# Optimization experiments

Hardware: AMD Instinct MI355X
Metric: run time of the kernel (lower is better)

## Reference

```python
import jax, jax.numpy as jnp
import numpy as np

N_NODES = 50000
N_EDGES = 500000
H_DIM = 128
BN_EPS = 1e-5


def setup_inputs() -> dict:
    key = jax.random.key(0)
    k1, k2, k3, k4 = jax.random.split(key, 4)
    ent_emb = jax.random.normal(k1, (N_NODES, H_DIM), dtype=jnp.float32)
    neigh_w = jax.random.normal(k2, (H_DIM, H_DIM), dtype=jnp.float32) * 0.05
    gamma = jnp.ones((H_DIM,), dtype=jnp.float32)
    beta = jnp.zeros((H_DIM,), dtype=jnp.float32)
    src = jax.random.randint(k3, (N_EDGES,), 0, N_NODES, dtype=jnp.int32)
    dst = jax.random.randint(k4, (N_EDGES,), 0, N_NODES, dtype=jnp.int32)
    return {"ent_emb": ent_emb, "neigh_w": neigh_w, "gamma": gamma,
            "beta": beta, "src": src, "dst": dst}


def reference(ent_emb, neigh_w, gamma, beta, src, dst):
    # u_dot_v: per-edge dot product of src and dst node embeddings -> [E]
    e_src = ent_emb[src]                      # [E, D] gather
    scores = jnp.sum(e_src * ent_emb[dst], axis=-1)  # [E]

    # edge_softmax: softmax over incoming edges of each destination node
    seg_max = jax.ops.segment_max(scores, dst, num_segments=N_NODES)
    seg_max = jnp.where(jnp.isfinite(seg_max), seg_max, 0.0)  # empty nodes
    ex = jnp.exp(scores - seg_max[dst])
    denom = jax.ops.segment_sum(ex, dst, num_segments=N_NODES)
    norm = ex / denom[dst]                    # [E]

    # u_mul_e + sum: weighted scatter-sum of src embeddings into dst nodes
    neigh = jax.ops.segment_sum(e_src * norm[:, None], dst,
                                num_segments=N_NODES)  # [N, D]

    # linear + BatchNorm1d (training mode, batch stats) + tanh
    h = neigh @ neigh_w
    mu = jnp.mean(h, axis=0)
    var = jnp.var(h, axis=0)                  # biased, matches torch BN
    h = (h - mu) * jax.lax.rsqrt(var + BN_EPS) * gamma + beta
    return jnp.tanh(h)
```

## Files before the change

### kernel.cpp

```cpp
#include <hip/hip_runtime.h>
#include <hip/hip_bf16.h>
#include <math.h>

#define N_NODES 50000
#define N_EDGES 500000
#define H_DIM   128
#define BN_EPS  1e-5f
#define GEMM_GRID ((N_NODES + 31) / 32)
#define SCAN_NBLK ((N_NODES + 255) / 256)
#define RED_NBLK  64

__global__ __launch_bounds__(256) void hist_kernel(
    const int* __restrict__ dst, int* __restrict__ deg)
{
    int e = blockIdx.x * blockDim.x + threadIdx.x;
    if (e < N_EDGES) atomicAdd(&deg[dst[e]], 1);
}

__global__ __launch_bounds__(256) void scan_partial_kernel(
    const int* __restrict__ deg, int* __restrict__ blocksum)
{
    __shared__ int red[256];
    int t = threadIdx.x;
    int i = blockIdx.x * 256 + t;
    red[t] = (i < N_NODES) ? deg[i] : 0;
    __syncthreads();
    #pragma unroll
    for (int off = 128; off; off >>= 1) {
        if (t < off) red[t] += red[t + off];
        __syncthreads();
    }
    if (t == 0) blocksum[blockIdx.x] = red[0];
}

__global__ __launch_bounds__(256) void scan_final_kernel(
    const int* __restrict__ deg, const int* __restrict__ blocksum,
    int* __restrict__ rowptr, int* __restrict__ cursor)
{
    __shared__ int bs[256];
    __shared__ int s[256];
    int t = threadIdx.x;

    bs[t] = (t < SCAN_NBLK) ? blocksum[t] : 0;
    __syncthreads();
    for (int off = 1; off < 256; off <<= 1) {
        int v = (t >= off) ? bs[t - off] : 0;
        __syncthreads();
        bs[t] += v;
        __syncthreads();
    }
    int blockoff = (blockIdx.x == 0) ? 0 : bs[blockIdx.x - 1];

    int i = blockIdx.x * 256 + t;
    int v = (i < N_NODES) ? deg[i] : 0;
    s[t] = v;
    __syncthreads();
    for (int off = 1; off < 256; off <<= 1) {
        int u = (t >= off) ? s[t - off] : 0;
        __syncthreads();
        s[t] += u;
        __syncthreads();
    }
    int excl = s[t] - v + blockoff;
    if (i < N_NODES) {
        rowptr[i] = excl;
        cursor[i] = excl;
        if (i == N_NODES - 1) rowptr[N_NODES] = excl + v;
    }
}

__global__ __launch_bounds__(256) void csr_scatter_kernel(
    const int* __restrict__ src, const int* __restrict__ dst,
    int* __restrict__ cursor, int* __restrict__ csr_src)
{
    int e = blockIdx.x * blockDim.x + threadIdx.x;
    if (e >= N_EDGES) return;
    int pos = atomicAdd(&cursor[dst[e]], 1);
    csr_src[pos] = src[e];
}

__global__ __launch_bounds__(256) void node_aggregate_kernel(
    const float* __restrict__ emb,
    const int* __restrict__ rowptr,
    const int* __restrict__ csr_src,
    float* __restrict__ neigh)
{
    int node = blockIdx.x * 8 + (threadIdx.x >> 5);
    int lane = threadIdx.x & 31;
    if (node >= N_NODES) return;

    int beg = rowptr[node];
    int end = rowptr[node + 1];

    const float4 b = *((const float4*)(emb + (size_t)node * H_DIM) + lane);

    float m = -INFINITY;
    float denom = 0.f;
    float4 acc = {0.f, 0.f, 0.f, 0.f};

    int e = beg;

    for (; e + 8 <= end; e += 8) {
        float4 a[8];
        float  p[8];
        #pragma unroll
        for (int u = 0; u < 8; ++u) {
            int s = csr_src[e + u];
            a[u] = *((const float4*)(emb + (size_t)s * H_DIM) + lane);
        }
        #pragma unroll
        for (int u = 0; u < 8; ++u)
            p[u] = a[u].x * b.x + a[u].y * b.y + a[u].z * b.z + a[u].w * b.w;
        #pragma unroll
        for (int off = 16; off; off >>= 1) {
            #pragma unroll
            for (int u = 0; u < 8; ++u)
                p[u] += __shfl_xor(p[u], off);
        }
        float mn = m;
        #pragma unroll
        for (int u = 0; u < 8; ++u) mn = fmaxf(mn, p[u]);
        float corr = __expf(m - mn);
        float w[8];
        #pragma unroll
        for (int u = 0; u < 8; ++u) w[u] = __expf(p[u] - mn);
        float ws = 0.f;
        #pragma unroll
        for (int u = 0; u < 8; ++u) ws += w[u];
        denom = denom * corr + ws;
        float sx = 0.f, sy = 0.f, sz = 0.f, sw = 0.f;
        #pragma unroll
        for (int u = 0; u < 8; ++u) {
            sx += a[u].x * w[u];
            sy += a[u].y * w[u];
            sz += a[u].z * w[u];
            sw += a[u].w * w[u];
        }
        acc.x = acc.x * corr + sx;
        acc.y = acc.y * corr + sy;
        acc.z = acc.z * corr + sz;
        acc.w = acc.w * corr + sw;
        m = mn;
    }

    if (e + 4 <= end) {
        float4 a[4];
        float  p[4];
        #pragma unroll
        for (int u = 0; u < 4; ++u) {
            int s = csr_src[e + u];
            a[u] = *((const float4*)(emb + (size_t)s * H_DIM) + lane);
        }
        #pragma unroll
        for (int u = 0; u < 4; ++u)
            p[u] = a[u].x * b.x + a[u].y * b.y + a[u].z * b.z + a[u].w * b.w;
        #pragma unroll
        for (int off = 16; off; off >>= 1) {
            #pragma unroll
            for (int u = 0; u < 4; ++u)
                p[u] += __shfl_xor(p[u], off);
        }
        float mn = fmaxf(fmaxf(fmaxf(p[0], p[1]), fmaxf(p[2], p[3])), m);
        float corr = __expf(m - mn);
        float w[4];
        #pragma unroll
        for (int u = 0; u < 4; ++u) w[u] = __expf(p[u] - mn);
        denom = denom * corr + w[0] + w[1] + w[2] + w[3];
        acc.x = acc.x * corr + a[0].x*w[0] + a[1].x*w[1] + a[2].x*w[2] + a[3].x*w[3];
        acc.y = acc.y * corr + a[0].y*w[0] + a[1].y*w[1] + a[2].y*w[2] + a[3].y*w[3];
        acc.z = acc.z * corr + a[0].z*w[0] + a[1].z*w[1] + a[2].z*w[2] + a[3].z*w[3];
        acc.w = acc.w * corr + a[0].w*w[0] + a[1].w*w[1] + a[2].w*w[2] + a[3].w*w[3];
        m = mn;
        e += 4;
    }

    for (; e < end; ++e) {
        int s = csr_src[e];
        float4 a = *((const float4*)(emb + (size_t)s * H_DIM) + lane);
        float p = a.x * b.x + a.y * b.y + a.z * b.z + a.w * b.w;
        #pragma unroll
        for (int off = 16; off; off >>= 1)
            p += __shfl_xor(p, off);
        float mn   = fmaxf(m, p);
        float corr = __expf(m - mn);
        float w    = __expf(p - mn);
        denom = denom * corr + w;
        acc.x = acc.x * corr + a.x * w;
        acc.y = acc.y * corr + a.y * w;
        acc.z = acc.z * corr + a.z * w;
        acc.w = acc.w * corr + a.w * w;
        m = mn;
    }

    float inv = (end > beg) ? (1.0f / denom) : 0.f;
    float4 o = {acc.x * inv, acc.y * inv, acc.z * inv, acc.w * inv};
    *((float4*)(neigh + (size_t)node * H_DIM) + lane) = o;
}

__global__ __launch_bounds__(256) void gemm_stats_kernel(
    const float* __restrict__ neigh,
    const float* __restrict__ W,
    float* __restrict__ h,
    float* __restrict__ partial)
{
    __shared__ float Ws[32][128];
    __shared__ float As[32][128];

    int t  = threadIdx.x;
    int tx = t & 31;
    int ty = t >> 5;
    int r0 = blockIdx.x * 32;

    const float4 z4 = {0.f, 0.f, 0.f, 0.f};
    for (int i = t; i < 32 * 32; i += 256) {
        int r = i >> 5, c4 = i & 31;
        int gr = r0 + r;
        float4 v = (gr < N_NODES) ? ((const float4*)(neigh + (size_t)gr * H_DIM))[c4] : z4;
        *(float4*)(&As[r][c4 * 4]) = v;
    }

    float acc[4][4];
    #pragma unroll
    for (int i = 0; i < 4; ++i)
        #pragma unroll
        for (int j = 0; j < 4; ++j)
            acc[i][j] = 0.f;

    for (int ks = 0; ks < 4; ++ks) {
        __syncthreads();
        for (int i = t; i < 32 * 32; i += 256) {
            int kk = i >> 5, c4 = i & 31;
            *(float4*)(&Ws[kk][c4 * 4]) =
                ((const float4*)(W + (size_t)(ks * 32 + kk) * H_DIM))[c4];
        }
        __syncthreads();

        #pragma unroll 8
        for (int kk = 0; kk < 32; ++kk) {
            float4 w = *(const float4*)(&Ws[kk][tx * 4]);
            int k = ks * 32 + kk;
            #pragma unroll
            for (int i = 0; i < 4; ++i) {
                float a = As[ty * 4 + i][k];
                acc[i][0] += a * w.x;
                acc[i][1] += a * w.y;
                acc[i][2] += a * w.z;
                acc[i][3] += a * w.w;
            }
        }
    }

    float csum[4] = {0.f, 0.f, 0.f, 0.f};
    float csq[4]  = {0.f, 0.f, 0.f, 0.f};

    #pragma unroll
    for (int i = 0; i < 4; ++i) {
        int gr = r0 + ty * 4 + i;
        if (gr < N_NODES) {
            float4 out;
            out.x = acc[i][0]; out.y = acc[i][1];
            out.z = acc[i][2]; out.w = acc[i][3];
            *(float4*)(h + (size_t)gr * H_DIM + tx * 4) = out;
            #pragma unroll
            for (int j = 0; j < 4; ++j) {
                csum[j] += acc[i][j];
                csq[j]  += acc[i][j] * acc[i][j];
            }
        }
    }

    __syncthreads();
    float* red = &As[0][0];
    #pragma unroll
    for (int j = 0; j < 4; ++j) {
        red[(tx * 8 + j) * 9 + ty]     = csum[j];
        red[(tx * 8 + 4 + j) * 9 + ty] = csq[j];
    }
    __syncthreads();
    float s = 0.f;
    #pragma unroll
    for (int q = 0; q < 8; ++q)
        s += red[t * 9 + q];
    partial[(size_t)blockIdx.x * 256 + t] = s;
}

__global__ __launch_bounds__(256) void reduce_partials_kernel(
    const float* __restrict__ partial, float* __restrict__ partial2)
{
    int t = threadIdx.x;
    int g = blockIdx.x;
    float s = 0.f;
    for (int b = g; b < GEMM_GRID; b += RED_NBLK)
        s += partial[(size_t)b * 256 + t];
    partial2[(size_t)g * 256 + t] = s;
}

__global__ __launch_bounds__(1024) void bn_stats_kernel(
    const float* __restrict__ partial2,
    const float* __restrict__ gamma,
    const float* __restrict__ beta,
    float* __restrict__ scale,
    float* __restrict__ shift)
{
    __shared__ float tot[4][256];
    __shared__ float tot2[256];
    int v = threadIdx.x & 255;
    int q = threadIdx.x >> 8;
    float s = 0.f;
    for (int b = q; b < RED_NBLK; b += 4)
        s += partial2[(size_t)b * 256 + v];
    tot[q][v] = s;
    __syncthreads();
    if (threadIdx.x < 256)
        tot2[v] = tot[0][v] + tot[1][v] + tot[2][v] + tot[3][v];
    __syncthreads();
    if (threadIdx.x < 128) {
        int c = threadIdx.x;
        int base = (c >> 2) * 8 + (c & 3);
        float cs = tot2[base];
        float cq = tot2[base + 4];
        const float invN = 1.0f / (float)N_NODES;
        float mu  = cs * invN;
        float var = cq * invN - mu * mu;
        float sc  = gamma[c] * rsqrtf(var + BN_EPS);
        scale[c] = sc;
        shift[c] = beta[c] - mu * sc;
    }
}

__global__ __launch_bounds__(256) void bn_tanh_kernel(
    float* __restrict__ h,
    const float* __restrict__ scale,
    const float* __restrict__ shift)
{
    size_t i = (size_t)blockIdx.x * blockDim.x + threadIdx.x;
    size_t idx4 = i * 4;
    if (idx4 >= (size_t)N_NODES * H_DIM) return;
    int c = (int)(idx4 & (H_DIM - 1));
    float4 v = *(float4*)(h + idx4);
    v.x = tanhf(v.x * scale[c + 0] + shift[c + 0]);
    v.y = tanhf(v.y * scale[c + 1] + shift[c + 1]);
    v.z = tanhf(v.z * scale[c + 2] + shift[c + 2]);
    v.w = tanhf(v.w * scale[c + 3] + shift[c + 3]);
    *(float4*)(h + idx4) = v;
}

extern "C" void kernel_launch(void* const* d_in, const int* in_sizes, int n_in,
                              void* d_out, int out_size, void* d_ws, size_t ws_size,
                              hipStream_t stream)
{
    const float* ent_emb = (const float*)d_in[0];
    const float* neigh_w = (const float*)d_in[1];
    const float* gamma   = (const float*)d_in[2];
    const float* beta    = (const float*)d_in[3];
    const int*   src     = (const int*)d_in[4];
    const int*   dst     = (const int*)d_in[5];
    float* out = (float*)d_out;

    char* ws = (char*)d_ws;
    float* neigh    = (float*)ws;
    int*   deg      = (int*)(ws + (size_t)N_NODES * H_DIM * 4);
    int*   rowptr   = deg + N_NODES;
    int*   cursor   = rowptr + N_NODES + 1;
    int*   csr_src  = cursor + N_NODES;
    int*   blocksum = csr_src + N_EDGES;
    float* partial  = (float*)(blocksum + SCAN_NBLK);
    float* partial2 = partial + (size_t)GEMM_GRID * 256;
    float* scale    = partial2 + (size_t)RED_NBLK * 256;
    float* shift    = scale + H_DIM;

    hipMemsetAsync(deg, 0, N_NODES * sizeof(int), stream);

    hist_kernel<<<(N_EDGES + 255) / 256, 256, 0, stream>>>(dst, deg);
    scan_partial_kernel<<<SCAN_NBLK, 256, 0, stream>>>(deg, blocksum);
    scan_final_kernel<<<SCAN_NBLK, 256, 0, stream>>>(deg, blocksum, rowptr, cursor);
    csr_scatter_kernel<<<(N_EDGES + 255) / 256, 256, 0, stream>>>(src, dst, cursor, csr_src);

    node_aggregate_kernel<<<(N_NODES + 7) / 8, 256, 0, stream>>>(
        ent_emb, rowptr, csr_src, neigh);

    gemm_stats_kernel<<<GEMM_GRID, 256, 0, stream>>>(neigh, neigh_w, out, partial);
    reduce_partials_kernel<<<RED_NBLK, 256, 0, stream>>>(partial, partial2);
    bn_stats_kernel<<<1, 1024, 0, stream>>>(partial2, gamma, beta, scale, shift);
    {
        size_t total4 = (size_t)N_NODES * H_DIM / 4;
        int blocks = (int)((total4 + 255) / 256);
        bn_tanh_kernel<<<blocks, 256, 0, stream>>>(out, scale, shift);
    }
}
```

Baseline: 171.5 us.

## Use bf16 MFMA for the node GEMM with swizzled LDS tiles

Replaces the FP32 scalar-FMA GEMM in the fused GEMM+stats kernel with bf16 MFMA 16x16x32 instructions. A small pre-kernel converts the weight matrix to transposed bf16, and activation tiles are converted to bf16 while being loaded into XOR-swizzled shared memory. The partial-stats layout changes to a plain column-ordered sum/sumsq layout, and bn_stats indexing is updated to match. This trades FP32 accuracy for bf16 inputs, which may move results relative to the reference, and it adds an extra kernel launch.

```diff
diff --git a/kernel.cpp b/kernel.cpp
--- a/kernel.cpp
+++ b/kernel.cpp
@@ -9,6 +9,25 @@
 #define GEMM_GRID ((N_NODES + 31) / 32)
 #define SCAN_NBLK ((N_NODES + 255) / 256)
 #define RED_NBLK  64
+
+typedef __attribute__((ext_vector_type(8))) short short8;
+typedef __attribute__((ext_vector_type(4))) float floatx4;
+
+__device__ __forceinline__ ushort f2bf(float x)
+{
+    unsigned u = __float_as_uint(x);
+    unsigned r = (u + 0x7FFFu + ((u >> 16) & 1u)) >> 16;
+    return (ushort)r;
+}
+
+__global__ __launch_bounds__(256) void cvt_w_kernel(
+    const float* __restrict__ W, ushort* __restrict__ wt)
+{
+    int i = blockIdx.x * 256 + threadIdx.x;
+    if (i >= H_DIM * H_DIM) return;
+    int k = i >> 7, c = i & 127;
+    wt[c * 128 + k] = f2bf(W[i]);
+}
 
 __global__ __launch_bounds__(256) void hist_kernel(
     const int* __restrict__ dst, int* __restrict__ deg)
@@ -199,88 +218,89 @@
 
 __global__ __launch_bounds__(256) void gemm_stats_kernel(
     const float* __restrict__ neigh,
-    const float* __restrict__ W,
+    const ushort* __restrict__ wt,
     float* __restrict__ h,
     float* __restrict__ partial)
 {
-    __shared__ float Ws[32][128];
-    __shared__ float As[32][128];
+    __shared__ ushort A_s[32 * 128];
+    __shared__ ushort W_s[128 * 128];
+    __shared__ float  red_s[128 * 9];
+    __shared__ float  red_q[128 * 9];
 
     int t  = threadIdx.x;
-    int tx = t & 31;
-    int ty = t >> 5;
     int r0 = blockIdx.x * 32;
 
-    const float4 z4 = {0.f, 0.f, 0.f, 0.f};
-    for (int i = t; i < 32 * 32; i += 256) {
-        int r = i >> 5, c4 = i & 31;
+    for (int g = t; g < 32 * 16; g += 256) {
+        int r = g >> 4, gc = g & 15;
         int gr = r0 + r;
-        float4 v = (gr < N_NODES) ? ((const float4*)(neigh + (size_t)gr * H_DIM))[c4] : z4;
-        *(float4*)(&As[r][c4 * 4]) = v;
-    }
-
-    float acc[4][4];
+        float4 x0 = {0.f,0.f,0.f,0.f}, x1 = {0.f,0.f,0.f,0.f};
+        if (gr < N_NODES) {
+            const float4* p = (const float4*)(neigh + (size_t)gr * H_DIM + gc * 8);
+            x0 = p[0]; x1 = p[1];
+        }
+        ushort v[8] = {f2bf(x0.x), f2bf(x0.y), f2bf(x0.z), f2bf(x0.w),
+                       f2bf(x1.x), f2bf(x1.y), f2bf(x1.z), f2bf(x1.w)};
+        int idx = r * 128 + ((gc * 8) ^ ((r & 7) << 3));
+        *(short8*)&A_s[idx] = *(short8*)v;
+    }
+    for (int g = t; g < 128 * 16; g += 256) {
+        int c = g >> 4, gk = g & 15;
+        short8 v = *(const short8*)(wt + (size_t)c * 128 + gk * 8);
+        int idx = c * 128 + ((gk * 8) ^ ((c & 7) << 3));
+        *(short8*)&W_s[idx] = v;
+    }
+    __syncthreads();
+
+    int w    = t >> 6;
+    int lane = t & 63;
+    int rbase = (w >> 1) * 16;
+    int c0    = (w & 1) * 64;
+    int l15   = lane & 15;
+    int kgrp  = lane >> 4;
+    int arow  = rbase + l15;
+    int k0l   = kgrp * 8;
+
+    floatx4 acc[4] = {{0.f,0.f,0.f,0.f},{0.f,0.f,0.f,0.f},
+                      {0.f,0.f,0.f,0.f},{0.f,0.f,0.f,0.f}};
+
     #pragma unroll
-    for (int i = 0; i < 4; ++i)
-        #pragma unroll
-        for (int j = 0; j < 4; ++j)
-            acc[i][j] = 0.f;
-
     for (int ks = 0; ks < 4; ++ks) {
-        __syncthreads();
-        for (int i = t; i < 32 * 32; i += 256) {
-            int kk = i >> 5, c4 = i & 31;
-            *(float4*)(&Ws[kk][c4 * 4]) =
-                ((const float4*)(W + (size_t)(ks * 32 + kk) * H_DIM))[c4];
-        }
-        __syncthreads();
-
-        #pragma unroll 8
-        for (int kk = 0; kk < 32; ++kk) {
-            float4 w = *(const float4*)(&Ws[kk][tx * 4]);
-            int k = ks * 32 + kk;
-            #pragma unroll
-            for (int i = 0; i < 4; ++i) {
-                float a = As[ty * 4 + i][k];
-                acc[i][0] += a * w.x;
-                acc[i][1] += a * w.y;
-                acc[i][2] += a * w.z;
-                acc[i][3] += a * w.w;
-            }
-        }
-    }
-
-    float csum[4] = {0.f, 0.f, 0.f, 0.f};
-    float csq[4]  = {0.f, 0.f, 0.f, 0.f};
-
+        int k0 = ks * 32 + k0l;
+        short8 af = *(const short8*)&A_s[arow * 128 + (k0 ^ ((arow & 7) << 3))];
+        #pragma unroll
+        for (int ct = 0; ct < 4; ++ct) {
+            int col = c0 + ct * 16 + l15;
+            short8 bf = *(const short8*)&W_s[col * 128 + (k0 ^ ((col & 7) << 3))];
+            acc[ct] = __builtin_amdgcn_mfma_f32_16x16x32_bf16(af, bf, acc[ct], 0, 0, 0);
+        }
+    }
+
+    int contrib = (w >> 1) * 4 + kgrp;
     #pragma unroll
-    for (int i = 0; i < 4; ++i) {
-        int gr = r0 + ty * 4 + i;
-        if (gr < N_NODES) {
-            float4 out;
-            out.x = acc[i][0]; out.y = acc[i][1];
-            out.z = acc[i][2]; out.w = acc[i][3];
-            *(float4*)(h + (size_t)gr * H_DIM + tx * 4) = out;
-            #pragma unroll
-            for (int j = 0; j < 4; ++j) {
-                csum[j] += acc[i][j];
-                csq[j]  += acc[i][j] * acc[i][j];
-            }
-        }
-    }
-
-    __syncthreads();
-    float* red = &As[0][0];
-    #pragma unroll
-    for (int j = 0; j < 4; ++j) {
-        red[(tx * 8 + j) * 9 + ty]     = csum[j];
-        red[(tx * 8 + 4 + j) * 9 + ty] = csq[j];
-    }
-    __syncthreads();
+    for (int ct = 0; ct < 4; ++ct) {
+        int col = c0 + ct * 16 + l15;
+        float ps = 0.f, pq = 0.f;
+        #pragma unroll
+        for (int reg = 0; reg < 4; ++reg) {
+            float v = acc[ct][reg];
+            int gr = r0 + rbase + kgrp * 4 + reg;
+            if (gr < N_NODES) h[(size_t)gr * H_DIM + col] = v;
+            ps += v;
+            pq += v * v;
+        }
+        red_s[col * 9 + contrib] = ps;
+        red_q[col * 9 + contrib] = pq;
+    }
+    __syncthreads();
+
     float s = 0.f;
-    #pragma unroll
-    for (int q = 0; q < 8; ++q)
-        s += red[t * 9 + q];
+    if (t < 128) {
+        #pragma unroll
+        for (int q = 0; q < 8; ++q) s += red_s[t * 9 + q];
+    } else {
+        #pragma unroll
+        for (int q = 0; q < 8; ++q) s += red_q[(t - 128) * 9 + q];
+    }
     partial[(size_t)blockIdx.x * 256 + t] = s;
 }
 
@@ -316,9 +336,8 @@
     __syncthreads();
     if (threadIdx.x < 128) {
         int c = threadIdx.x;
-        int base = (c >> 2) * 8 + (c & 3);
-        float cs = tot2[base];
-        float cq = tot2[base + 4];
+        float cs = tot2[c];
+        float cq = tot2[c + 128];
         const float invN = 1.0f / (float)N_NODES;
         float mu  = cs * invN;
         float var = cq * invN - mu * mu;
@@ -357,19 +376,21 @@
     const int*   dst     = (const int*)d_in[5];
     float* out = (float*)d_out;
 
-    char* ws = (char*)d_ws;
-    float* neigh    = (float*)ws;
-    int*   deg      = (int*)(ws + (size_t)N_NODES * H_DIM * 4);
-    int*   rowptr   = deg + N_NODES;
-    int*   cursor   = rowptr + N_NODES + 1;
-    int*   csr_src  = cursor + N_NODES;
-    int*   blocksum = csr_src + N_EDGES;
-    float* partial  = (float*)(blocksum + SCAN_NBLK);
-    float* partial2 = partial + (size_t)GEMM_GRID * 256;
-    float* scale    = partial2 + (size_t)RED_NBLK * 256;
-    float* shift    = scale + H_DIM;
+    float*  neigh    = (float*)d_ws;
+    int*    deg      = (int*)(neigh + (size_t)N_NODES * H_DIM);
+    int*    rowptr   = deg + N_NODES;
+    int*    cursor   = rowptr + N_NODES + 1;
+    int*    csr_src  = cursor + N_NODES;
+    int*    blocksum = csr_src + N_EDGES;
+    float*  partial  = (float*)(blocksum + SCAN_NBLK);
+    float*  partial2 = partial + (size_t)GEMM_GRID * 256;
+    ushort* wt       = (ushort*)(partial2 + (size_t)RED_NBLK * 256);
+    float*  scale    = (float*)(wt + H_DIM * H_DIM);
+    float*  shift    = scale + H_DIM;
 
     hipMemsetAsync(deg, 0, N_NODES * sizeof(int), stream);
+
+    cvt_w_kernel<<<(H_DIM * H_DIM + 255) / 256, 256, 0, stream>>>(neigh_w, wt);
 
     hist_kernel<<<(N_EDGES + 255) / 256, 256, 0, stream>>>(dst, deg);
     scan_partial_kernel<<<SCAN_NBLK, 256, 0, stream>>>(deg, blocksum);
@@ -379,7 +400,7 @@
     node_aggregate_kernel<<<(N_NODES + 7) / 8, 256, 0, stream>>>(
         ent_emb, rowptr, csr_src, neigh);
 
-    gemm_stats_kernel<<<GEMM_GRID, 256, 0, stream>>>(neigh, neigh_w, out, partial);
+    gemm_stats_kernel<<<GEMM_GRID, 256, 0, stream>>>(neigh, wt, out, partial);
     reduce_partials_kernel<<<RED_NBLK, 256, 0, stream>>>(partial, partial2);
     bn_stats_kernel<<<1, 1024, 0, stream>>>(partial2, gamma, beta, scale, shift);
     {
```

Result: faster. 156.4 us (-8.8%).
